# Performance work log

Measured on AMD Instinct MI355X. Metric: run time of the kernel, lower is better.

## Reference

```python
import jax, jax.numpy as jnp
import numpy as np

N = 50000
E = 800000
IN_DIM = 16
HID = 64
HEADS = 4
OUT_DIM = 2
LN_EPS = 1e-5
NEG_SLOPE = 0.2  # GATConv default negative_slope


def _layernorm(h, g, b):
    mu = jnp.mean(h, axis=-1, keepdims=True)
    var = jnp.var(h, axis=-1, keepdims=True)
    return (h - mu) * jax.lax.rsqrt(var + LN_EPS) * g + b


def _gat_layer(h, src, dst, w, a_src, a_dst, b):
    # PyG GATConv, concat=False: per-head channels C=HID, head-averaged output.
    n = h.shape[0]
    xp = (h @ w).reshape(n, HEADS, HID)          # [N,H,C]
    e_src = jnp.sum(xp * a_src, axis=-1)          # [N,H]
    e_dst = jnp.sum(xp * a_dst, axis=-1)          # [N,H]
    e = jax.nn.leaky_relu(e_src[src] + e_dst[dst], negative_slope=NEG_SLOPE)  # [Etot,H]
    # numerically-stable segment softmax over edges grouped by target node
    m = jax.lax.stop_gradient(jax.ops.segment_max(e, dst, num_segments=n))
    ex = jnp.exp(e - m[dst])
    denom = jax.ops.segment_sum(ex, dst, num_segments=n)
    alpha = ex / denom[dst]                       # [Etot,H]
    out = jax.ops.segment_sum(xp[src] * alpha[:, :, None], dst, num_segments=n)  # [N,H,C]
    return jnp.mean(out, axis=1) + b              # mean over heads (concat=False) + bias


def _forward(x, edge_index, w0, a_src0, a_dst0, b0, ln0_g, ln0_b,
             w1, a_src1, a_dst1, b1, ln1_g, ln1_b,
             gru_w_ih, gru_w_hh, gru_b_ih, gru_b_hh,
             d0_w, d0_b, d1_w, d1_b, d2_w, d2_b):
    n = x.shape[0]
    # add_self_loops=True
    loops = jnp.arange(n, dtype=edge_index.dtype)
    src = jnp.concatenate([edge_index[0], loops])
    dst = jnp.concatenate([edge_index[1], loops])
    # GAT layer 1 + LayerNorm + ReLU (dropout is identity in eval)
    h = _gat_layer(x, src, dst, w0, a_src0, a_dst0, b0)
    h = jax.nn.relu(_layernorm(h, ln0_g, ln0_b))
    # GAT layer 2 + LayerNorm (last layer -> no ReLU)
    h = _gat_layer(h, src, dst, w1, a_src1, a_dst1, b1)
    h = _layernorm(h, ln1_g, ln1_b)
    # single-timestep GRU with zero initial hidden state (PyTorch GRU cell math)
    h0 = jnp.zeros((n, HID), dtype=h.dtype)
    gi = h @ gru_w_ih.T + gru_b_ih
    gh = h0 @ gru_w_hh.T + gru_b_hh
    gi_r, gi_z, gi_n = jnp.split(gi, 3, axis=-1)
    gh_r, gh_z, gh_n = jnp.split(gh, 3, axis=-1)
    r = jax.nn.sigmoid(gi_r + gh_r)
    z = jax.nn.sigmoid(gi_z + gh_z)
    cand = jnp.tanh(gi_n + r * gh_n)
    temporal = (1.0 - z) * cand + z * h0
    # MLP decoder on cat([temporal_features, x])
    d = jnp.concatenate([temporal, x], axis=-1)
    d = jax.nn.relu(d @ d0_w + d0_b)
    d = jax.nn.relu(d @ d1_w + d1_b)
    d = d @ d2_w + d2_b
    return jnp.clip(d, -0.5, 0.5)


def setup_inputs():
    key = jax.random.key(0)
    ks = jax.random.split(key, 16)
    rn = lambda k, shape, s=0.05: jax.random.normal(k, shape, dtype=jnp.float32) * s
    return {
        'x': jax.random.normal(ks[0], (N, IN_DIM), dtype=jnp.float32),
        'edge_index': jax.random.randint(ks[1], (2, E), 0, N, dtype=jnp.int32),
        'w0': rn(ks[2], (IN_DIM, HEADS * HID)),
        'a_src0': rn(ks[3], (HEADS, HID)),
        'a_dst0': rn(ks[4], (HEADS, HID)),
        'b0': jnp.zeros((HID,), jnp.float32),
        'ln0_g': jnp.ones((HID,), jnp.float32),
        'ln0_b': jnp.zeros((HID,), jnp.float32),
        'w1': rn(ks[5], (HID, HEADS * HID)),
        'a_src1': rn(ks[6], (HEADS, HID)),
        'a_dst1': rn(ks[7], (HEADS, HID)),
        'b1': jnp.zeros((HID,), jnp.float32),
        'ln1_g': jnp.ones((HID,), jnp.float32),
        'ln1_b': jnp.zeros((HID,), jnp.float32),
        'gru_w_ih': rn(ks[8], (3 * HID, HID)),
        'gru_w_hh': rn(ks[9], (3 * HID, HID)),
        'gru_b_ih': jnp.zeros((3 * HID,), jnp.float32),
        'gru_b_hh': jnp.zeros((3 * HID,), jnp.float32),
        'd0_w': rn(ks[10], (HID + IN_DIM, HID)),
        'd0_b': jnp.zeros((HID,), jnp.float32),
        'd1_w': rn(ks[11], (HID, HID // 2)),
        'd1_b': jnp.zeros((HID // 2,), jnp.float32),
        'd2_w': rn(ks[12], (HID // 2, OUT_DIM)),
        'd2_b': jnp.zeros((OUT_DIM,), jnp.float32),
    }


def reference(x, edge_index, w0, a_src0, a_dst0, b0, ln0_g, ln0_b,
              w1, a_src1, a_dst1, b1, ln1_g, ln1_b,
              gru_w_ih, gru_w_hh, gru_b_ih, gru_b_hh,
              d0_w, d0_b, d1_w, d1_b, d2_w, d2_b):
    return _forward(x, edge_index, w0, a_src0, a_dst0, b0, ln0_g, ln0_b,
                    w1, a_src1, a_dst1, b1, ln1_g, ln1_b,
                    gru_w_ih, gru_w_hh, gru_b_ih, gru_b_hh,
                    d0_w, d0_b, d1_w, d1_b, d2_w, d2_b)
```

## Files before the change

kernel.cpp:

```cpp
#include <hip/hip_runtime.h>
#include <hip/hip_fp16.h>
#include <math.h>

#define NN 50000
#define NE 800000
#define ETOT (NE + NN)
#define HID 64
#define CH 256
#define IND 16
#define LN_EPS 1e-5f
#define NSLOPE 0.2f
#define SCB 49

__device__ __forceinline__ float lrelu(float v){ return v > 0.f ? v : NSLOPE * v; }
__device__ __forceinline__ float sigf(float v){ return 1.f / (1.f + __expf(-v)); }

__device__ __forceinline__ int block_excl_scan(int v, int t, int* wtot){
  const int lane = t & 63, w = t >> 6;
  int inc = v;
  #pragma unroll
  for (int d = 1; d < 64; d <<= 1){
    int tv = __shfl_up(inc, d);
    if (lane >= d) inc += tv;
  }
  if (lane == 63) wtot[w] = inc;
  __syncthreads();
  if (t == 0){
    int acc = 0;
    #pragma unroll
    for (int k = 0; k < 16; ++k){ int tv = wtot[k]; wtot[k] = acc; acc += tv; }
  }
  __syncthreads();
  return wtot[w] + inc - v;
}


__global__ void k_hist(const int* __restrict__ ei, int* __restrict__ deg){
  int e = blockIdx.x * 256 + threadIdx.x;
  if (e >= ETOT) return;
  int d = (e < NE) ? ei[NE + e] : (e - NE);
  atomicAdd(&deg[d], 1);
}

__global__ __launch_bounds__(1024) void k_scan_a(const int* __restrict__ deg,
                                                 int* __restrict__ bsum){
  __shared__ int wtot[16];
  const int t = threadIdx.x, lane = t & 63, w = t >> 6;
  const int i = blockIdx.x * 1024 + t;
  int v = (i < NN) ? deg[i] : 0;
  #pragma unroll
  for (int d = 32; d; d >>= 1) v += __shfl_xor(v, d);
  if (lane == 0) wtot[w] = v;
  __syncthreads();
  if (t == 0){
    int acc = 0;
    #pragma unroll
    for (int k = 0; k < 16; ++k) acc += wtot[k];
    bsum[blockIdx.x] = acc;
  }
}

__global__ __launch_bounds__(64) void k_scan_b(const int* __restrict__ bsum,
                                               int* __restrict__ boff){
  const int t = threadIdx.x;
  int v = (t < SCB) ? bsum[t] : 0;
  int inc = v;
  #pragma unroll
  for (int d = 1; d < 64; d <<= 1){
    int tv = __shfl_up(inc, d);
    if (t >= d) inc += tv;
  }
  if (t < SCB) boff[t] = inc - v;
}

__global__ __launch_bounds__(1024) void k_scan_c(const int* __restrict__ deg,
                                                 const int* __restrict__ boff,
                                                 int* __restrict__ rp,
                                                 int* __restrict__ cursor){
  __shared__ int wtot[16];
  const int t = threadIdx.x;
  const int i = blockIdx.x * 1024 + t;
  int v = (i < NN) ? deg[i] : 0;
  int excl = block_excl_scan(v, t, wtot) + boff[blockIdx.x];
  if (i < NN){ rp[i] = excl; cursor[i] = excl; }
  if (i == NN - 1) rp[NN] = excl + v;
}

__global__ void k_scatter(const int* __restrict__ ei, int* __restrict__ cursor,
                          int* __restrict__ col){
  int e = blockIdx.x * 256 + threadIdx.x;
  if (e >= ETOT) return;
  int s, d;
  if (e < NE){ s = ei[e]; d = ei[NE + e]; } else { s = d = e - NE; }
  int pos = atomicAdd(&cursor[d], 1);
  col[pos] = s;
}


template<int K>
__global__ __launch_bounds__(256) void k_proj(const float* __restrict__ h,
    const float* __restrict__ w, const float* __restrict__ asr,
    const float* __restrict__ adr, __half* __restrict__ xph,
    float* __restrict__ es, float* __restrict__ ed){
  __shared__ float w_s[K * CH];
  __shared__ float h_s[K][36];
  __shared__ float as_s[CH], ad_s[CH];
  const int t = threadIdx.x;
  for (int i = t; i < K * CH; i += 256) w_s[i] = w[i];
  as_s[t] = asr[t]; ad_s[t] = adr[t];
  const int wv = t >> 6, l = t & 63;
  const int tc = l & 31, th = l >> 5;
  const int g = wv * 2 + th;
  const int c0 = tc * 4;
  const int hA = tc >> 4;

  for (int tile = blockIdx.x * 32; tile < NN; tile += gridDim.x * 32){
    __syncthreads();
    for (int i = t; i < 32 * K; i += 256){
      int n = i / K, k = i % K;
      int nn = tile + n;
      h_s[k][n] = (nn < NN) ? h[nn * K + k] : 0.f;
    }
    __syncthreads();

    float acc[4][8];
    #pragma unroll
    for (int j = 0; j < 4; ++j)
      #pragma unroll
      for (int i = 0; i < 8; ++i) acc[j][i] = 0.f;

    #pragma unroll 4
    for (int k = 0; k < K; ++k){
      const float4 wa = *(const float4*)&w_s[k * CH + c0];
      const float4 wb = *(const float4*)&w_s[k * CH + c0 + 128];
      const float4 hv = *(const float4*)&h_s[k][g * 4];
      const float hj0 = hv.x, hj1 = hv.y, hj2 = hv.z, hj3 = hv.w;
      #define STEP(j, hjv) \
        acc[j][0] = fmaf(hjv, wa.x, acc[j][0]); \
        acc[j][1] = fmaf(hjv, wa.y, acc[j][1]); \
        acc[j][2] = fmaf(hjv, wa.z, acc[j][2]); \
        acc[j][3] = fmaf(hjv, wa.w, acc[j][3]); \
        acc[j][4] = fmaf(hjv, wb.x, acc[j][4]); \
        acc[j][5] = fmaf(hjv, wb.y, acc[j][5]); \
        acc[j][6] = fmaf(hjv, wb.z, acc[j][6]); \
        acc[j][7] = fmaf(hjv, wb.w, acc[j][7]);
      STEP(0, hj0) STEP(1, hj1) STEP(2, hj2) STEP(3, hj3)
      #undef STEP
    }

    #pragma unroll
    for (int j = 0; j < 4; ++j){
      const int nj = tile + g * 4 + j;
      float pa = 0.f, pb = 0.f, qa = 0.f, qb = 0.f;
      #pragma unroll
      for (int i = 0; i < 4; ++i){
        pa = fmaf(acc[j][i],     as_s[c0 + i],       pa);
        pb = fmaf(acc[j][4 + i], as_s[c0 + 128 + i], pb);
        qa = fmaf(acc[j][i],     ad_s[c0 + i],       qa);
        qb = fmaf(acc[j][4 + i], ad_s[c0 + 128 + i], qb);
      }
      #pragma unroll
      for (int d = 8; d; d >>= 1){
        pa += __shfl_xor(pa, d); pb += __shfl_xor(pb, d);
        qa += __shfl_xor(qa, d); qb += __shfl_xor(qb, d);
      }
      if (nj < NN){
        union { uint2 u; __half2 h2[2]; } oA, oB;
        oA.h2[0] = __float22half2_rn(make_float2(acc[j][0], acc[j][1]));
        oA.h2[1] = __float22half2_rn(make_float2(acc[j][2], acc[j][3]));
        oB.h2[0] = __float22half2_rn(make_float2(acc[j][4], acc[j][5]));
        oB.h2[1] = __float22half2_rn(make_float2(acc[j][6], acc[j][7]));
        *(uint2*)&xph[(size_t)nj * CH + c0]       = oA.u;
        *(uint2*)&xph[(size_t)nj * CH + c0 + 128] = oB.u;
        if ((tc & 15) == 0){
          es[nj * 4 + hA]     = pa;
          es[nj * 4 + hA + 2] = pb;
          ed[nj * 4 + hA]     = qa;
          ed[nj * 4 + hA + 2] = qb;
        }
      }
    }
  }
}


template<int DO_RELU>
__global__ __launch_bounds__(256) void k_agg(const __half* __restrict__ xph,
    const float4* __restrict__ es4, const float4* __restrict__ ed4,
    const int* __restrict__ rp, const int* __restrict__ col,
    const float* __restrict__ bias, const float* __restrict__ lng,
    const float* __restrict__ lnb, float* __restrict__ hout){
  __shared__ float pbuf[4][64][4];
  const int wid = threadIdx.x >> 6, lane = threadIdx.x & 63;
  const int n = blockIdx.x * 4 + wid;
  if (n >= NN) return;
  const int head = lane >> 4;
  const int c4 = lane * 4;
  const int beg = rp[n], end = rp[n + 1];
  const float4 edn = ed4[n];
  const __half* __restrict__ xpc = xph + c4;
  float den = 0.f;
  float ax = 0.f, ay = 0.f, az = 0.f, aw = 0.f;

  for (int base = beg; base < end; base += 64){
    const int cnt = min(end - base, 64);
    const int myS = col[base + min(lane, cnt - 1)];
    const float4 e = es4[myS];
    const bool act = lane < cnt;
    float4 p4;
    p4.x = act ? __expf(lrelu(e.x + edn.x)) : 0.f;
    p4.y = act ? __expf(lrelu(e.y + edn.y)) : 0.f;
    p4.z = act ? __expf(lrelu(e.z + edn.z)) : 0.f;
    p4.w = act ? __expf(lrelu(e.w + edn.w)) : 0.f;
    *(float4*)&pbuf[wid][lane][0] = p4;
    const int sOff = myS * CH;

    for (int u0 = 0; u0 < cnt; u0 += 8){
      float pw[8]; uint2 xv[8];
      #pragma unroll
      for (int u = 0; u < 8; ++u){
        const int so = __shfl(sOff, u0 + u);
        xv[u] = *(const uint2*)&xpc[(size_t)so];
        pw[u] = pbuf[wid][u0 + u][head];
      }
      #pragma unroll
      for (int u = 0; u < 8; ++u){
        union { uint2 u2; __half2 h2[2]; } cv; cv.u2 = xv[u];
        const float2 lo = __half22float2(cv.h2[0]);
        const float2 hi = __half22float2(cv.h2[1]);
        den += pw[u];
        ax = fmaf(lo.x, pw[u], ax); ay = fmaf(lo.y, pw[u], ay);
        az = fmaf(hi.x, pw[u], az); aw = fmaf(hi.y, pw[u], aw);
      }
    }
  }

  const float inv = 1.f / den;
  ax *= inv; ay *= inv; az *= inv; aw *= inv;
  #pragma unroll
  for (int d = 16; d <= 32; d <<= 1){
    ax += __shfl_xor(ax, d); ay += __shfl_xor(ay, d);
    az += __shfl_xor(az, d); aw += __shfl_xor(aw, d);
  }
  const int cc4 = (lane & 15) * 4;
  const float4 b4 = *(const float4*)&bias[cc4];
  ax = ax * 0.25f + b4.x; ay = ay * 0.25f + b4.y;
  az = az * 0.25f + b4.z; aw = aw * 0.25f + b4.w;
  float s = ax + ay + az + aw;
  float q = ax * ax + ay * ay + az * az + aw * aw;
  #pragma unroll
  for (int d = 8; d; d >>= 1){ s += __shfl_xor(s, d); q += __shfl_xor(q, d); }
  const float mu = s * (1.f / 64.f);
  const float var = q * (1.f / 64.f) - mu * mu;
  const float rs = rsqrtf(var + LN_EPS);
  const float4 g4 = *(const float4*)&lng[cc4];
  const float4 t4 = *(const float4*)&lnb[cc4];
  ax = (ax - mu) * rs * g4.x + t4.x; ay = (ay - mu) * rs * g4.y + t4.y;
  az = (az - mu) * rs * g4.z + t4.z; aw = (aw - mu) * rs * g4.w + t4.w;
  if (DO_RELU){
    ax = fmaxf(ax, 0.f); ay = fmaxf(ay, 0.f);
    az = fmaxf(az, 0.f); aw = fmaxf(aw, 0.f);
  }
  if (lane < 16){
    float4 o; o.x = ax; o.y = ay; o.z = az; o.w = aw;
    *(float4*)&hout[n * HID + cc4] = o;
  }
}


#define WTS 196

__global__ __launch_bounds__(256) void k_gru(const float* __restrict__ h,
    const float* __restrict__ wih, const float* __restrict__ bih,
    const float* __restrict__ bhh, float* __restrict__ tmp){
  __shared__ float wT[64 * WTS];
  __shared__ float h_s[64][34];
  __shared__ float bi_s[192], bh_s[192];
  const int t = threadIdx.x;
  for (int i = t; i < 192 * 64; i += 256){
    int c = i >> 6, k = i & 63;
    wT[k * WTS + c] = wih[i];
  }
  if (t < 192){ bi_s[t] = bih[t]; bh_s[t] = bhh[t]; }
  const int col = t & 15, gg = t >> 4;
  const int c0 = col * 4;

  for (int tile = blockIdx.x * 32; tile < NN; tile += gridDim.x * 32){
    __syncthreads();
    for (int i = t; i < 32 * 64; i += 256){
      int nidx = i >> 6, k = i & 63;
      int nn = tile + nidx;
      h_s[k][nidx] = (nn < NN) ? h[nn * 64 + k] : 0.f;
    }
    __syncthreads();

    float ar[2][4] = {{0}}, az[2][4] = {{0}}, an[2][4] = {{0}};
    #pragma unroll 4
    for (int k = 0; k < 64; ++k){
      const float4 wr = *(const float4*)&wT[k * WTS + c0];
      const float4 wz = *(const float4*)&wT[k * WTS + 64 + c0];
      const float4 wn = *(const float4*)&wT[k * WTS + 128 + c0];
      const float h0v = h_s[k][gg * 2];
      const float h1v = h_s[k][gg * 2 + 1];
      ar[0][0] = fmaf(h0v, wr.x, ar[0][0]); ar[0][1] = fmaf(h0v, wr.y, ar[0][1]);
      ar[0][2] = fmaf(h0v, wr.z, ar[0][2]); ar[0][3] = fmaf(h0v, wr.w, ar[0][3]);
      az[0][0] = fmaf(h0v, wz.x, az[0][0]); az[0][1] = fmaf(h0v, wz.y, az[0][1]);
      az[0][2] = fmaf(h0v, wz.z, az[0][2]); az[0][3] = fmaf(h0v, wz.w, az[0][3]);
      an[0][0] = fmaf(h0v, wn.x, an[0][0]); an[0][1] = fmaf(h0v, wn.y, an[0][1]);
      an[0][2] = fmaf(h0v, wn.z, an[0][2]); an[0][3] = fmaf(h0v, wn.w, an[0][3]);
      ar[1][0] = fmaf(h1v, wr.x, ar[1][0]); ar[1][1] = fmaf(h1v, wr.y, ar[1][1]);
      ar[1][2] = fmaf(h1v, wr.z, ar[1][2]); ar[1][3] = fmaf(h1v, wr.w, ar[1][3]);
      az[1][0] = fmaf(h1v, wz.x, az[1][0]); az[1][1] = fmaf(h1v, wz.y, az[1][1]);
      az[1][2] = fmaf(h1v, wz.z, az[1][2]); az[1][3] = fmaf(h1v, wz.w, az[1][3]);
      an[1][0] = fmaf(h1v, wn.x, an[1][0]); an[1][1] = fmaf(h1v, wn.y, an[1][1]);
      an[1][2] = fmaf(h1v, wn.z, an[1][2]); an[1][3] = fmaf(h1v, wn.w, an[1][3]);
    }

    #pragma unroll
    for (int j = 0; j < 2; ++j){
      const int nj = tile + gg * 2 + j;
      if (nj < NN){
        float tv[4];
        #pragma unroll
        for (int i = 0; i < 4; ++i){
          const int c = c0 + i;
          const float r  = sigf(ar[j][i] + bi_s[c] + bh_s[c]);
          const float zz = sigf(az[j][i] + bi_s[64 + c] + bh_s[64 + c]);
          const float cd = tanhf(an[j][i] + bi_s[128 + c] + r * bh_s[128 + c]);
          tv[i] = (1.f - zz) * cd;
        }
        float4 o; o.x = tv[0]; o.y = tv[1]; o.z = tv[2]; o.w = tv[3];
        *(float4*)&tmp[(size_t)nj * 64 + c0] = o;
      }
    }
  }
}


__global__ __launch_bounds__(256) void k_dec(const float* __restrict__ tmp,
    const float* __restrict__ x, const float* __restrict__ d0w,
    const float* __restrict__ d0b, const float* __restrict__ d1w,
    const float* __restrict__ d1b, const float* __restrict__ d2w,
    const float* __restrict__ d2b, float* __restrict__ out){
  __shared__ float w0s[80 * 64];
  __shared__ float w1s[64 * 32];
  __shared__ float w2s[64];
  __shared__ float b0s[64], b1s[32], b2s[2];
  __shared__ float dc[80][34];
  __shared__ float t0s[64][34];
  __shared__ float t1s[32][34];
  const int t = threadIdx.x;
  for (int i = t; i < 80 * 64; i += 256) w0s[i] = d0w[i];
  for (int i = t; i < 64 * 32; i += 256) w1s[i] = d1w[i];
  if (t < 64) w2s[t] = d2w[t];
  if (t < 64) b0s[t] = d0b[t];
  if (t < 32) b1s[t] = d1b[t];
  if (t < 2)  b2s[t] = d2b[t];

  for (int tile = blockIdx.x * 32; tile < NN; tile += gridDim.x * 32){
    __syncthreads();
    for (int i = t; i < 32 * 64; i += 256){
      int nidx = i >> 6, k = i & 63;
      int nn = tile + nidx;
      dc[k][nidx] = (nn < NN) ? tmp[(size_t)nn * 64 + k] : 0.f;
    }
    for (int i = t; i < 32 * 16; i += 256){
      int nidx = i >> 4, k = i & 15;
      int nn = tile + nidx;
      dc[64 + k][nidx] = (nn < NN) ? x[nn * IND + k] : 0.f;
    }
    __syncthreads();

    {
      const int col = t & 15, gg = t >> 4;
      const int c0 = col * 4;
      float a[2][4] = {{0}};
      #pragma unroll 4
      for (int k = 0; k < 80; ++k){
        const float4 wv = *(const float4*)&w0s[k * 64 + c0];
        const float b0v = dc[k][gg * 2];
        const float b1v = dc[k][gg * 2 + 1];
        a[0][0] = fmaf(b0v, wv.x, a[0][0]); a[0][1] = fmaf(b0v, wv.y, a[0][1]);
        a[0][2] = fmaf(b0v, wv.z, a[0][2]); a[0][3] = fmaf(b0v, wv.w, a[0][3]);
        a[1][0] = fmaf(b1v, wv.x, a[1][0]); a[1][1] = fmaf(b1v, wv.y, a[1][1]);
        a[1][2] = fmaf(b1v, wv.z, a[1][2]); a[1][3] = fmaf(b1v, wv.w, a[1][3]);
      }
      #pragma unroll
      for (int j = 0; j < 2; ++j)
        #pragma unroll
        for (int i = 0; i < 4; ++i)
          t0s[c0 + i][gg * 2 + j] = fmaxf(a[j][i] + b0s[c0 + i], 0.f);
    }
    __syncthreads();

    {
      const int col = t & 7, gg = t >> 3;
      const int c0 = col * 4;
      float a[4] = {0, 0, 0, 0};
      #pragma unroll 4
      for (int k = 0; k < 64; ++k){
        const float4 wv = *(const float4*)&w1s[k * 32 + c0];
        const float bv = t0s[k][gg];
        a[0] = fmaf(bv, wv.x, a[0]); a[1] = fmaf(bv, wv.y, a[1]);
        a[2] = fmaf(bv, wv.z, a[2]); a[3] = fmaf(bv, wv.w, a[3]);
      }
      #pragma unroll
      for (int i = 0; i < 4; ++i)
        t1s[c0 + i][gg] = fmaxf(a[i] + b1s[c0 + i], 0.f);
    }
    __syncthreads();

    if (t < 64){
      const int nidx = t >> 1, o = t & 1;
      float a = b2s[o];
      #pragma unroll
      for (int k = 0; k < 32; ++k) a = fmaf(t1s[k][nidx], w2s[k * 2 + o], a);
      const int nn = tile + nidx;
      if (nn < NN) out[nn * 2 + o] = fminf(fmaxf(a, -0.5f), 0.5f);
    }
  }
}


extern "C" void kernel_launch(void* const* d_in, const int* in_sizes, int n_in,
                              void* d_out, int out_size, void* d_ws, size_t ws_size,
                              hipStream_t stream){
  (void)in_sizes; (void)n_in; (void)out_size; (void)ws_size;
  const float* x      = (const float*)d_in[0];
  const int*   ei     = (const int*)d_in[1];
  const float* w0     = (const float*)d_in[2];
  const float* as0    = (const float*)d_in[3];
  const float* ad0    = (const float*)d_in[4];
  const float* b0     = (const float*)d_in[5];
  const float* ln0g   = (const float*)d_in[6];
  const float* ln0b   = (const float*)d_in[7];
  const float* w1     = (const float*)d_in[8];
  const float* as1    = (const float*)d_in[9];
  const float* ad1    = (const float*)d_in[10];
  const float* b1     = (const float*)d_in[11];
  const float* ln1g   = (const float*)d_in[12];
  const float* ln1b   = (const float*)d_in[13];
  const float* wih    = (const float*)d_in[14];
  const float* bih    = (const float*)d_in[16];
  const float* bhh    = (const float*)d_in[17];
  const float* d0w    = (const float*)d_in[18];
  const float* d0b    = (const float*)d_in[19];
  const float* d1w    = (const float*)d_in[20];
  const float* d1b    = (const float*)d_in[21];
  const float* d2w    = (const float*)d_in[22];
  const float* d2b    = (const float*)d_in[23];
  float* outp = (float*)d_out;

  char* ws = (char*)d_ws;
  size_t o = 0;
  auto alloc = [&](size_t bytes) -> char* {
    char* r = ws + o;
    o += (bytes + 255) & ~(size_t)255;
    return r;
  };
  int*    deg    = (int*)   alloc(NN * sizeof(int));
  int*    rp     = (int*)   alloc((NN + 1) * sizeof(int));
  int*    cursor = (int*)   alloc(NN * sizeof(int));
  int*    col    = (int*)   alloc((size_t)ETOT * sizeof(int));
  int*    bsum   = (int*)   alloc(SCB * sizeof(int));
  int*    boff   = (int*)   alloc(SCB * sizeof(int));
  float*  es     = (float*) alloc((size_t)NN * 4 * sizeof(float));
  float*  ed     = (float*) alloc((size_t)NN * 4 * sizeof(float));
  __half* xph    = (__half*)alloc((size_t)NN * CH * sizeof(__half));
  float*  hbuf   = (float*) alloc((size_t)NN * HID * sizeof(float));
  float*  tmp    = (float*) alloc((size_t)NN * HID * sizeof(float));

  hipMemsetAsync(deg, 0, NN * sizeof(int), stream);
  k_hist<<<(ETOT + 255) / 256, 256, 0, stream>>>(ei, deg);
  k_scan_a<<<SCB, 1024, 0, stream>>>(deg, bsum);
  k_scan_b<<<1, 64, 0, stream>>>(bsum, boff);
  k_scan_c<<<SCB, 1024, 0, stream>>>(deg, boff, rp, cursor);
  k_scatter<<<(ETOT + 255) / 256, 256, 0, stream>>>(ei, cursor, col);
  k_proj<IND><<<(NN + 31) / 32, 256, 0, stream>>>(x, w0, as0, ad0, xph, es, ed);
  k_agg<1><<<(NN + 3) / 4, 256, 0, stream>>>(xph, (const float4*)es,
                                             (const float4*)ed, rp, col,
                                             b0, ln0g, ln0b, hbuf);
  k_proj<HID><<<(NN + 31) / 32, 256, 0, stream>>>(hbuf, w1, as1, ad1, xph, es, ed);
  k_agg<0><<<(NN + 3) / 4, 256, 0, stream>>>(xph, (const float4*)es,
                                             (const float4*)ed, rp, col,
                                             b1, ln1g, ln1b, hbuf);
  k_gru<<<(NN + 31) / 32, 256, 0, stream>>>(hbuf, wih, bih, bhh, tmp);
  k_dec<<<(NN + 31) / 32, 256, 0, stream>>>(tmp, x, d0w, d0b, d1w, d1b, d2w, d2b,
                                            outp);
}
```

Before: 350.4 us.

## Process two nodes per wavefront in aggregation and fuse GRU with decoder

The aggregation kernel now assigns each half-wavefront to one node, with each lane gathering 8 fp16 channels (16-byte loads) instead of 4. This is meant to improve lane utilisation on low-degree nodes and widen memory transactions. The GRU and decoder kernels are merged into one kernel that keeps the GRU output in shared memory, removing a full N×64 intermediate write and read plus one launch. GRU and decoder weights are stored as fp16 in shared memory, which adds rounding error to the head layers. Paired nodes in a wavefront loop to the larger of their two degrees, so imbalanced pairs waste work.

After: 349.8 us. No clear change (-0.2%).

```diff
diff --git a/kernel.cpp b/kernel.cpp
--- a/kernel.cpp
+++ b/kernel.cpp
@@ -190,234 +190,232 @@
     const int* __restrict__ rp, const int* __restrict__ col,
     const float* __restrict__ bias, const float* __restrict__ lng,
     const float* __restrict__ lnb, float* __restrict__ hout){
-  __shared__ float pbuf[4][64][4];
+  __shared__ float pbuf[4][2][32][4];
   const int wid = threadIdx.x >> 6, lane = threadIdx.x & 63;
-  const int n = blockIdx.x * 4 + wid;
-  if (n >= NN) return;
-  const int head = lane >> 4;
-  const int c4 = lane * 4;
-  const int beg = rp[n], end = rp[n + 1];
+  const int half = lane >> 5, l32 = lane & 31;
+  const int n = blockIdx.x * 8 + wid * 2 + half;
+  const int head = l32 >> 3;
+  const int c8 = l32 * 8;
+  const int beg = rp[n];
+  const int deg = rp[n + 1] - beg;
+  const int dmax = max(deg, __shfl(deg, lane ^ 32));
   const float4 edn = ed4[n];
-  const __half* __restrict__ xpc = xph + c4;
   float den = 0.f;
-  float ax = 0.f, ay = 0.f, az = 0.f, aw = 0.f;
-
-  for (int base = beg; base < end; base += 64){
-    const int cnt = min(end - base, 64);
-    const int myS = col[base + min(lane, cnt - 1)];
+  float acc[8];
+  #pragma unroll
+  for (int i = 0; i < 8; ++i) acc[i] = 0.f;
+
+  for (int base = 0; base < dmax; base += 32){
+    const int cmax = min(dmax - base, 32);
+    const int myS = col[beg + min(base + l32, deg - 1)];
     const float4 e = es4[myS];
-    const bool act = lane < cnt;
+    const bool act = (base + l32 < deg);
     float4 p4;
     p4.x = act ? __expf(lrelu(e.x + edn.x)) : 0.f;
     p4.y = act ? __expf(lrelu(e.y + edn.y)) : 0.f;
     p4.z = act ? __expf(lrelu(e.z + edn.z)) : 0.f;
     p4.w = act ? __expf(lrelu(e.w + edn.w)) : 0.f;
-    *(float4*)&pbuf[wid][lane][0] = p4;
+    *(float4*)&pbuf[wid][half][l32][0] = p4;
     const int sOff = myS * CH;
 
-    for (int u0 = 0; u0 < cnt; u0 += 8){
-      float pw[8]; uint2 xv[8];
+    for (int u0 = 0; u0 < cmax; u0 += 8){
+      float pw[8]; uint4 xv[8];
       #pragma unroll
       for (int u = 0; u < 8; ++u){
-        const int so = __shfl(sOff, u0 + u);
-        xv[u] = *(const uint2*)&xpc[(size_t)so];
-        pw[u] = pbuf[wid][u0 + u][head];
+        const int uu = u0 + u, us = uu & 31;
+        const int so = __shfl(sOff, (lane & 32) + us);
+        xv[u] = *(const uint4*)&xph[so + c8];
+        pw[u] = (uu < cmax) ? pbuf[wid][half][us][head] : 0.f;
       }
       #pragma unroll
       for (int u = 0; u < 8; ++u){
-        union { uint2 u2; __half2 h2[2]; } cv; cv.u2 = xv[u];
-        const float2 lo = __half22float2(cv.h2[0]);
-        const float2 hi = __half22float2(cv.h2[1]);
+        union { uint4 q; __half2 h2[4]; } cv; cv.q = xv[u];
+        const float2 f0 = __half22float2(cv.h2[0]);
+        const float2 f1 = __half22float2(cv.h2[1]);
+        const float2 f2 = __half22float2(cv.h2[2]);
+        const float2 f3 = __half22float2(cv.h2[3]);
         den += pw[u];
-        ax = fmaf(lo.x, pw[u], ax); ay = fmaf(lo.y, pw[u], ay);
-        az = fmaf(hi.x, pw[u], az); aw = fmaf(hi.y, pw[u], aw);
+        acc[0] = fmaf(f0.x, pw[u], acc[0]); acc[1] = fmaf(f0.y, pw[u], acc[1]);
+        acc[2] = fmaf(f1.x, pw[u], acc[2]); acc[3] = fmaf(f1.y, pw[u], acc[3]);
+        acc[4] = fmaf(f2.x, pw[u], acc[4]); acc[5] = fmaf(f2.y, pw[u], acc[5]);
+        acc[6] = fmaf(f3.x, pw[u], acc[6]); acc[7] = fmaf(f3.y, pw[u], acc[7]);
       }
     }
   }
 
   const float inv = 1.f / den;
-  ax *= inv; ay *= inv; az *= inv; aw *= inv;
-  #pragma unroll
-  for (int d = 16; d <= 32; d <<= 1){
-    ax += __shfl_xor(ax, d); ay += __shfl_xor(ay, d);
-    az += __shfl_xor(az, d); aw += __shfl_xor(aw, d);
-  }
-  const int cc4 = (lane & 15) * 4;
-  const float4 b4 = *(const float4*)&bias[cc4];
-  ax = ax * 0.25f + b4.x; ay = ay * 0.25f + b4.y;
-  az = az * 0.25f + b4.z; aw = aw * 0.25f + b4.w;
-  float s = ax + ay + az + aw;
-  float q = ax * ax + ay * ay + az * az + aw * aw;
-  #pragma unroll
-  for (int d = 8; d; d >>= 1){ s += __shfl_xor(s, d); q += __shfl_xor(q, d); }
+  #pragma unroll
+  for (int i = 0; i < 8; ++i) acc[i] *= inv;
+  #pragma unroll
+  for (int i = 0; i < 8; ++i){
+    acc[i] += __shfl_xor(acc[i], 8);
+    acc[i] += __shfl_xor(acc[i], 16);
+  }
+  const int ch0 = (l32 & 7) * 8;
+  const float4 bA = *(const float4*)&bias[ch0];
+  const float4 bB = *(const float4*)&bias[ch0 + 4];
+  acc[0] = acc[0]*0.25f + bA.x; acc[1] = acc[1]*0.25f + bA.y;
+  acc[2] = acc[2]*0.25f + bA.z; acc[3] = acc[3]*0.25f + bA.w;
+  acc[4] = acc[4]*0.25f + bB.x; acc[5] = acc[5]*0.25f + bB.y;
+  acc[6] = acc[6]*0.25f + bB.z; acc[7] = acc[7]*0.25f + bB.w;
+  float s = 0.f, q = 0.f;
+  #pragma unroll
+  for (int i = 0; i < 8; ++i){ s += acc[i]; q += acc[i]*acc[i]; }
+  #pragma unroll
+  for (int d = 4; d; d >>= 1){ s += __shfl_xor(s, d); q += __shfl_xor(q, d); }
   const float mu = s * (1.f / 64.f);
   const float var = q * (1.f / 64.f) - mu * mu;
   const float rs = rsqrtf(var + LN_EPS);
-  const float4 g4 = *(const float4*)&lng[cc4];
-  const float4 t4 = *(const float4*)&lnb[cc4];
-  ax = (ax - mu) * rs * g4.x + t4.x; ay = (ay - mu) * rs * g4.y + t4.y;
-  az = (az - mu) * rs * g4.z + t4.z; aw = (aw - mu) * rs * g4.w + t4.w;
+  const float4 gA = *(const float4*)&lng[ch0];
+  const float4 gB = *(const float4*)&lng[ch0 + 4];
+  const float4 tA = *(const float4*)&lnb[ch0];
+  const float4 tB = *(const float4*)&lnb[ch0 + 4];
+  acc[0] = (acc[0]-mu)*rs*gA.x + tA.x; acc[1] = (acc[1]-mu)*rs*gA.y + tA.y;
+  acc[2] = (acc[2]-mu)*rs*gA.z + tA.z; acc[3] = (acc[3]-mu)*rs*gA.w + tA.w;
+  acc[4] = (acc[4]-mu)*rs*gB.x + tB.x; acc[5] = (acc[5]-mu)*rs*gB.y + tB.y;
+  acc[6] = (acc[6]-mu)*rs*gB.z + tB.z; acc[7] = (acc[7]-mu)*rs*gB.w + tB.w;
   if (DO_RELU){
-    ax = fmaxf(ax, 0.f); ay = fmaxf(ay, 0.f);
-    az = fmaxf(az, 0.f); aw = fmaxf(aw, 0.f);
-  }
-  if (lane < 16){
-    float4 o; o.x = ax; o.y = ay; o.z = az; o.w = aw;
-    *(float4*)&hout[n * HID + cc4] = o;
-  }
-}
-
-
-#define WTS 196
-
-__global__ __launch_bounds__(256) void k_gru(const float* __restrict__ h,
-    const float* __restrict__ wih, const float* __restrict__ bih,
-    const float* __restrict__ bhh, float* __restrict__ tmp){
-  __shared__ float wT[64 * WTS];
+    #pragma unroll
+    for (int i = 0; i < 8; ++i) acc[i] = fmaxf(acc[i], 0.f);
+  }
+  if (l32 < 8){
+    float4 oA, oB;
+    oA.x = acc[0]; oA.y = acc[1]; oA.z = acc[2]; oA.w = acc[3];
+    oB.x = acc[4]; oB.y = acc[5]; oB.z = acc[6]; oB.w = acc[7];
+    *(float4*)&hout[n * HID + l32 * 8]     = oA;
+    *(float4*)&hout[n * HID + l32 * 8 + 4] = oB;
+  }
+}
+
+
+__global__ __launch_bounds__(256) void k_head(const float* __restrict__ h,
+    const float* __restrict__ x, const float* __restrict__ wih,
+    const float* __restrict__ bih, const float* __restrict__ bhh,
+    const float* __restrict__ d0w, const float* __restrict__ d0b,
+    const float* __restrict__ d1w, const float* __restrict__ d1b,
+    const float* __restrict__ d2w, const float* __restrict__ d2b,
+    float* __restrict__ out){
+  __shared__ __half wT[64 * 196];
+  __shared__ __half w0s[80 * 64];
+  __shared__ __half w1s[64 * 32];
+  __shared__ float w2s[64];
+  __shared__ float bi_s[192], bh_s[192], b0s[64], b1s[32], b2s[2];
   __shared__ float h_s[64][34];
-  __shared__ float bi_s[192], bh_s[192];
-  const int t = threadIdx.x;
-  for (int i = t; i < 192 * 64; i += 256){
-    int c = i >> 6, k = i & 63;
-    wT[k * WTS + c] = wih[i];
-  }
-  if (t < 192){ bi_s[t] = bih[t]; bh_s[t] = bhh[t]; }
-  const int col = t & 15, gg = t >> 4;
-  const int c0 = col * 4;
-
-  for (int tile = blockIdx.x * 32; tile < NN; tile += gridDim.x * 32){
-    __syncthreads();
-    for (int i = t; i < 32 * 64; i += 256){
-      int nidx = i >> 6, k = i & 63;
-      int nn = tile + nidx;
-      h_s[k][nidx] = (nn < NN) ? h[nn * 64 + k] : 0.f;
-    }
-    __syncthreads();
-
-    float ar[2][4] = {{0}}, az[2][4] = {{0}}, an[2][4] = {{0}};
-    #pragma unroll 4
-    for (int k = 0; k < 64; ++k){
-      const float4 wr = *(const float4*)&wT[k * WTS + c0];
-      const float4 wz = *(const float4*)&wT[k * WTS + 64 + c0];
-      const float4 wn = *(const float4*)&wT[k * WTS + 128 + c0];
-      const float h0v = h_s[k][gg * 2];
-      const float h1v = h_s[k][gg * 2 + 1];
-      ar[0][0] = fmaf(h0v, wr.x, ar[0][0]); ar[0][1] = fmaf(h0v, wr.y, ar[0][1]);
-      ar[0][2] = fmaf(h0v, wr.z, ar[0][2]); ar[0][3] = fmaf(h0v, wr.w, ar[0][3]);
-      az[0][0] = fmaf(h0v, wz.x, az[0][0]); az[0][1] = fmaf(h0v, wz.y, az[0][1]);
-      az[0][2] = fmaf(h0v, wz.z, az[0][2]); az[0][3] = fmaf(h0v, wz.w, az[0][3]);
-      an[0][0] = fmaf(h0v, wn.x, an[0][0]); an[0][1] = fmaf(h0v, wn.y, an[0][1]);
-      an[0][2] = fmaf(h0v, wn.z, an[0][2]); an[0][3] = fmaf(h0v, wn.w, an[0][3]);
-      ar[1][0] = fmaf(h1v, wr.x, ar[1][0]); ar[1][1] = fmaf(h1v, wr.y, ar[1][1]);
-      ar[1][2] = fmaf(h1v, wr.z, ar[1][2]); ar[1][3] = fmaf(h1v, wr.w, ar[1][3]);
-      az[1][0] = fmaf(h1v, wz.x, az[1][0]); az[1][1] = fmaf(h1v, wz.y, az[1][1]);
-      az[1][2] = fmaf(h1v, wz.z, az[1][2]); az[1][3] = fmaf(h1v, wz.w, az[1][3]);
-      an[1][0] = fmaf(h1v, wn.x, an[1][0]); an[1][1] = fmaf(h1v, wn.y, an[1][1]);
-      an[1][2] = fmaf(h1v, wn.z, an[1][2]); an[1][3] = fmaf(h1v, wn.w, an[1][3]);
-    }
-
-    #pragma unroll
-    for (int j = 0; j < 2; ++j){
-      const int nj = tile + gg * 2 + j;
-      if (nj < NN){
-        float tv[4];
-        #pragma unroll
-        for (int i = 0; i < 4; ++i){
-          const int c = c0 + i;
-          const float r  = sigf(ar[j][i] + bi_s[c] + bh_s[c]);
-          const float zz = sigf(az[j][i] + bi_s[64 + c] + bh_s[64 + c]);
-          const float cd = tanhf(an[j][i] + bi_s[128 + c] + r * bh_s[128 + c]);
-          tv[i] = (1.f - zz) * cd;
-        }
-        float4 o; o.x = tv[0]; o.y = tv[1]; o.z = tv[2]; o.w = tv[3];
-        *(float4*)&tmp[(size_t)nj * 64 + c0] = o;
-      }
-    }
-  }
-}
-
-
-__global__ __launch_bounds__(256) void k_dec(const float* __restrict__ tmp,
-    const float* __restrict__ x, const float* __restrict__ d0w,
-    const float* __restrict__ d0b, const float* __restrict__ d1w,
-    const float* __restrict__ d1b, const float* __restrict__ d2w,
-    const float* __restrict__ d2b, float* __restrict__ out){
-  __shared__ float w0s[80 * 64];
-  __shared__ float w1s[64 * 32];
-  __shared__ float w2s[64];
-  __shared__ float b0s[64], b1s[32], b2s[2];
   __shared__ float dc[80][34];
   __shared__ float t0s[64][34];
   __shared__ float t1s[32][34];
   const int t = threadIdx.x;
-  for (int i = t; i < 80 * 64; i += 256) w0s[i] = d0w[i];
-  for (int i = t; i < 64 * 32; i += 256) w1s[i] = d1w[i];
+  for (int i = t; i < 192 * 64; i += 256)
+    wT[(i & 63) * 196 + (i >> 6)] = __float2half(wih[i]);
+  for (int i = t; i < 80 * 64; i += 256) w0s[i] = __float2half(d0w[i]);
+  for (int i = t; i < 64 * 32; i += 256) w1s[i] = __float2half(d1w[i]);
   if (t < 64) w2s[t] = d2w[t];
+  if (t < 192){ bi_s[t] = bih[t]; bh_s[t] = bhh[t]; }
   if (t < 64) b0s[t] = d0b[t];
   if (t < 32) b1s[t] = d1b[t];
   if (t < 2)  b2s[t] = d2b[t];
 
-  for (int tile = blockIdx.x * 32; tile < NN; tile += gridDim.x * 32){
-    __syncthreads();
-    for (int i = t; i < 32 * 64; i += 256){
-      int nidx = i >> 6, k = i & 63;
-      int nn = tile + nidx;
-      dc[k][nidx] = (nn < NN) ? tmp[(size_t)nn * 64 + k] : 0.f;
-    }
-    for (int i = t; i < 32 * 16; i += 256){
-      int nidx = i >> 4, k = i & 15;
-      int nn = tile + nidx;
-      dc[64 + k][nidx] = (nn < NN) ? x[nn * IND + k] : 0.f;
-    }
-    __syncthreads();
-
-    {
-      const int col = t & 15, gg = t >> 4;
-      const int c0 = col * 4;
-      float a[2][4] = {{0}};
-      #pragma unroll 4
-      for (int k = 0; k < 80; ++k){
-        const float4 wv = *(const float4*)&w0s[k * 64 + c0];
-        const float b0v = dc[k][gg * 2];
-        const float b1v = dc[k][gg * 2 + 1];
-        a[0][0] = fmaf(b0v, wv.x, a[0][0]); a[0][1] = fmaf(b0v, wv.y, a[0][1]);
-        a[0][2] = fmaf(b0v, wv.z, a[0][2]); a[0][3] = fmaf(b0v, wv.w, a[0][3]);
-        a[1][0] = fmaf(b1v, wv.x, a[1][0]); a[1][1] = fmaf(b1v, wv.y, a[1][1]);
-        a[1][2] = fmaf(b1v, wv.z, a[1][2]); a[1][3] = fmaf(b1v, wv.w, a[1][3]);
-      }
-      #pragma unroll
-      for (int j = 0; j < 2; ++j)
-        #pragma unroll
-        for (int i = 0; i < 4; ++i)
-          t0s[c0 + i][gg * 2 + j] = fmaxf(a[j][i] + b0s[c0 + i], 0.f);
-    }
-    __syncthreads();
-
-    {
-      const int col = t & 7, gg = t >> 3;
-      const int c0 = col * 4;
-      float a[4] = {0, 0, 0, 0};
-      #pragma unroll 4
-      for (int k = 0; k < 64; ++k){
-        const float4 wv = *(const float4*)&w1s[k * 32 + c0];
-        const float bv = t0s[k][gg];
-        a[0] = fmaf(bv, wv.x, a[0]); a[1] = fmaf(bv, wv.y, a[1]);
-        a[2] = fmaf(bv, wv.z, a[2]); a[3] = fmaf(bv, wv.w, a[3]);
-      }
+  const int tile = blockIdx.x * 32;
+  for (int i = t; i < 32 * 64; i += 256){
+    int nidx = i >> 6, k = i & 63;
+    int nn = tile + nidx;
+    h_s[k][nidx] = (nn < NN) ? h[nn * 64 + k] : 0.f;
+  }
+  for (int i = t; i < 32 * 16; i += 256){
+    int nidx = i >> 4, k = i & 15;
+    int nn = tile + nidx;
+    dc[64 + k][nidx] = (nn < NN) ? x[nn * IND + k] : 0.f;
+  }
+  __syncthreads();
+
+  const int col = t & 15, gg = t >> 4, c0 = col * 4;
+  {
+    float ar[2][4] = {{0}}, az[2][4] = {{0}}, an[2][4] = {{0}};
+    #pragma unroll 4
+    for (int k = 0; k < 64; ++k){
+      union { uint2 u; __half2 h2[2]; } R, Z, N_;
+      R.u  = *(const uint2*)&wT[k * 196 + c0];
+      Z.u  = *(const uint2*)&wT[k * 196 + 64 + c0];
+      N_.u = *(const uint2*)&wT[k * 196 + 128 + c0];
+      const float2 r01 = __half22float2(R.h2[0]),  r23 = __half22float2(R.h2[1]);
+      const float2 z01 = __half22float2(Z.h2[0]),  z23 = __half22float2(Z.h2[1]);
+      const float2 n01 = __half22float2(N_.h2[0]), n23 = __half22float2(N_.h2[1]);
+      const float h0v = h_s[k][gg * 2];
+      const float h1v = h_s[k][gg * 2 + 1];
+      ar[0][0] = fmaf(h0v, r01.x, ar[0][0]); ar[0][1] = fmaf(h0v, r01.y, ar[0][1]);
+      ar[0][2] = fmaf(h0v, r23.x, ar[0][2]); ar[0][3] = fmaf(h0v, r23.y, ar[0][3]);
+      az[0][0] = fmaf(h0v, z01.x, az[0][0]); az[0][1] = fmaf(h0v, z01.y, az[0][1]);
+      az[0][2] = fmaf(h0v, z23.x, az[0][2]); az[0][3] = fmaf(h0v, z23.y, az[0][3]);
+      an[0][0] = fmaf(h0v, n01.x, an[0][0]); an[0][1] = fmaf(h0v, n01.y, an[0][1]);
+      an[0][2] = fmaf(h0v, n23.x, an[0][2]); an[0][3] = fmaf(h0v, n23.y, an[0][3]);
+      ar[1][0] = fmaf(h1v, r01.x, ar[1][0]); ar[1][1] = fmaf(h1v, r01.y, ar[1][1]);
+      ar[1][2] = fmaf(h1v, r23.x, ar[1][2]); ar[1][3] = fmaf(h1v, r23.y, ar[1][3]);
+      az[1][0] = fmaf(h1v, z01.x, az[1][0]); az[1][1] = fmaf(h1v, z01.y, az[1][1]);
+      az[1][2] = fmaf(h1v, z23.x, az[1][2]); az[1][3] = fmaf(h1v, z23.y, az[1][3]);
+      an[1][0] = fmaf(h1v, n01.x, an[1][0]); an[1][1] = fmaf(h1v, n01.y, an[1][1]);
+      an[1][2] = fmaf(h1v, n23.x, an[1][2]); an[1][3] = fmaf(h1v, n23.y, an[1][3]);
+    }
+    #pragma unroll
+    for (int j = 0; j < 2; ++j){
+      #pragma unroll
+      for (int i = 0; i < 4; ++i){
+        const int c = c0 + i;
+        const float r  = sigf(ar[j][i] + bi_s[c] + bh_s[c]);
+        const float zz = sigf(az[j][i] + bi_s[64 + c] + bh_s[64 + c]);
+        const float cd = tanhf(an[j][i] + bi_s[128 + c] + r * bh_s[128 + c]);
+        dc[c][gg * 2 + j] = (1.f - zz) * cd;
+      }
+    }
+  }
+  __syncthreads();
+
+  {
+    float a[2][4] = {{0}};
+    #pragma unroll 4
+    for (int k = 0; k < 80; ++k){
+      union { uint2 u; __half2 h2[2]; } W;
+      W.u = *(const uint2*)&w0s[k * 64 + c0];
+      const float2 w01 = __half22float2(W.h2[0]), w23 = __half22float2(W.h2[1]);
+      const float b0v = dc[k][gg * 2];
+      const float b1v = dc[k][gg * 2 + 1];
+      a[0][0] = fmaf(b0v, w01.x, a[0][0]); a[0][1] = fmaf(b0v, w01.y, a[0][1]);
+      a[0][2] = fmaf(b0v, w23.x, a[0][2]); a[0][3] = fmaf(b0v, w23.y, a[0][3]);
+      a[1][0] = fmaf(b1v, w01.x, a[1][0]); a[1][1] = fmaf(b1v, w01.y, a[1][1]);
+      a[1][2] = fmaf(b1v, w23.x, a[1][2]); a[1][3] = fmaf(b1v, w23.y, a[1][3]);
+    }
+    #pragma unroll
+    for (int j = 0; j < 2; ++j)
       #pragma unroll
       for (int i = 0; i < 4; ++i)
-        t1s[c0 + i][gg] = fmaxf(a[i] + b1s[c0 + i], 0.f);
-    }
-    __syncthreads();
-
-    if (t < 64){
-      const int nidx = t >> 1, o = t & 1;
-      float a = b2s[o];
-      #pragma unroll
-      for (int k = 0; k < 32; ++k) a = fmaf(t1s[k][nidx], w2s[k * 2 + o], a);
-      const int nn = tile + nidx;
-      if (nn < NN) out[nn * 2 + o] = fminf(fmaxf(a, -0.5f), 0.5f);
-    }
+        t0s[c0 + i][gg * 2 + j] = fmaxf(a[j][i] + b0s[c0 + i], 0.f);
+  }
+  __syncthreads();
+
+  {
+    const int c1 = (t & 7) * 4, g1 = t >> 3;
+    float a[4] = {0, 0, 0, 0};
+    #pragma unroll 4
+    for (int k = 0; k < 64; ++k){
+      union { uint2 u; __half2 h2[2]; } W;
+      W.u = *(const uint2*)&w1s[k * 32 + c1];
+      const float2 w01 = __half22float2(W.h2[0]), w23 = __half22float2(W.h2[1]);
+      const float bv = t0s[k][g1];
+      a[0] = fmaf(bv, w01.x, a[0]); a[1] = fmaf(bv, w01.y, a[1]);
+      a[2] = fmaf(bv, w23.x, a[2]); a[3] = fmaf(bv, w23.y, a[3]);
+    }
+    #pragma unroll
+    for (int i = 0; i < 4; ++i)
+      t1s[c1 + i][g1] = fmaxf(a[i] + b1s[c1 + i], 0.f);
+  }
+  __syncthreads();
+
+  if (t < 64){
+    const int nidx = t >> 1, o = t & 1;
+    float a = b2s[o];
+    #pragma unroll
+    for (int k = 0; k < 32; ++k) a = fmaf(t1s[k][nidx], w2s[k * 2 + o], a);
+    const int nn = tile + nidx;
+    if (nn < NN) out[nn * 2 + o] = fminf(fmaxf(a, -0.5f), 0.5f);
   }
 }
 
@@ -468,7 +466,6 @@
   float*  ed     = (float*) alloc((size_t)NN * 4 * sizeof(float));
   __half* xph    = (__half*)alloc((size_t)NN * CH * sizeof(__half));
   float*  hbuf   = (float*) alloc((size_t)NN * HID * sizeof(float));
-  float*  tmp    = (float*) alloc((size_t)NN * HID * sizeof(float));
 
   hipMemsetAsync(deg, 0, NN * sizeof(int), stream);
   k_hist<<<(ETOT + 255) / 256, 256, 0, stream>>>(ei, deg);
@@ -477,14 +474,11 @@
   k_scan_c<<<SCB, 1024, 0, stream>>>(deg, boff, rp, cursor);
   k_scatter<<<(ETOT + 255) / 256, 256, 0, stream>>>(ei, cursor, col);
   k_proj<IND><<<(NN + 31) / 32, 256, 0, stream>>>(x, w0, as0, ad0, xph, es, ed);
-  k_agg<1><<<(NN + 3) / 4, 256, 0, stream>>>(xph, (const float4*)es,
-                                             (const float4*)ed, rp, col,
-                                             b0, ln0g, ln0b, hbuf);
+  k_agg<1><<<NN / 8, 256, 0, stream>>>(xph, (const float4*)es, (const float4*)ed,
+                                       rp, col, b0, ln0g, ln0b, hbuf);
   k_proj<HID><<<(NN + 31) / 32, 256, 0, stream>>>(hbuf, w1, as1, ad1, xph, es, ed);
-  k_agg<0><<<(NN + 3) / 4, 256, 0, stream>>>(xph, (const float4*)es,
-                                             (const float4*)ed, rp, col,
-                                             b1, ln1g, ln1b, hbuf);
-  k_gru<<<(NN + 31) / 32, 256, 0, stream>>>(hbuf, wih, bih, bhh, tmp);
-  k_dec<<<(NN + 31) / 32, 256, 0, stream>>>(tmp, x, d0w, d0b, d1w, d1b, d2w, d2b,
-                                            outp);
-}
+  k_agg<0><<<NN / 8, 256, 0, stream>>>(xph, (const float4*)es, (const float4*)ed,
+                                       rp, col, b1, ln1g, ln1b, hbuf);
+  k_head<<<(NN + 31) / 32, 256, 0, stream>>>(hbuf, x, wih, bih, bhh,
+                                             d0w, d0b, d1w, d1b, d2w, d2b, outp);
+}
```
